# Kernel tuning notes

Measured on AMD Instinct MI355X. Metric: run time of the kernel, lower is better.

Reference implementation:

```python
import jax, jax.numpy as jnp
import numpy as np

N = 50000   # num nodes
E = 800000  # num edges
D = 128     # embedding dim
EPS = 1e-5


def setup_inputs() -> dict:
    key = jax.random.key(0)
    ks = jax.random.split(key, 16)
    x = jnp.arange(N, dtype=jnp.int32)
    edge_index = jax.random.randint(ks[0], (2, E), 0, N, dtype=jnp.int32)
    weight = jax.random.uniform(ks[1], (E,), dtype=jnp.float32)
    emb = jax.random.normal(ks[2], (N, D), dtype=jnp.float32)
    # layer dims: 128->128, 128->64, 64->32
    dims = [(128, 128), (128, 64), (64, 32)]
    inp = {"x": x, "edge_index": edge_index, "weight": weight, "emb": emb}
    for i, (fi, fo) in enumerate(dims, start=1):
        s = 1.0 / np.sqrt(fi)
        inp[f"W{i}"] = jax.random.uniform(ks[3 * i], (fi, fo), dtype=jnp.float32, minval=-s, maxval=s)
        inp[f"b{i}"] = jnp.zeros((fo,), dtype=jnp.float32)
        inp[f"g{i}"] = jnp.ones((fo,), dtype=jnp.float32)
        inp[f"be{i}"] = jnp.zeros((fo,), dtype=jnp.float32)
    return inp


def _gcn_conv(h, src, dst, w, W, b):
    # PyG GCNConv: linear, add self-loops (weight 1), symmetric normalization, scatter-add
    h = h @ W  # [N, Fout]
    loop = jnp.arange(N, dtype=src.dtype)
    src_l = jnp.concatenate([src, loop])
    dst_l = jnp.concatenate([dst, loop])
    w_l = jnp.concatenate([w, jnp.ones((N,), w.dtype)])
    deg = jax.ops.segment_sum(w_l, dst_l, num_segments=N)
    dinv = jnp.where(deg > 0, jax.lax.rsqrt(jnp.maximum(deg, 1e-30)), 0.0)
    norm = dinv[src_l] * w_l * dinv[dst_l]  # [E+N]
    msg = h[src_l] * norm[:, None]          # gather + scale, [E+N, Fout]
    out = jax.ops.segment_sum(msg, dst_l, num_segments=N)
    return out + b


def _batch_norm(h, g, be):
    mu = h.mean(axis=0)
    var = h.var(axis=0)  # biased, as torch BN uses for normalization
    return (h - mu) * jax.lax.rsqrt(var + EPS) * g + be


def reference(x, edge_index, weight, emb,
              W1, b1, g1, be1,
              W2, b2, g2, be2,
              W3, b3, g3, be3):
    src, dst = edge_index[0], edge_index[1]
    h = emb[x]  # embedding lookup
    h = _batch_norm(_gcn_conv(h, src, dst, weight, W1, b1), g1, be1)
    h = jax.nn.relu(h)
    h = _batch_norm(_gcn_conv(h, src, dst, weight, W2, b2), g2, be2)
    h = jax.nn.relu(h)
    h = _batch_norm(_gcn_conv(h, src, dst, weight, W3, b3), g3, be3)
    return h
```

## Files before the change

kernel.cpp:

```cpp
#include <hip/hip_runtime.h>
#include <hip/hip_bf16.h>

#define BN_EPS 1e-5f
#define FIXSCALE 16777216.0f
#define FIXINV   5.9604644775390625e-08
#define LOWMASK  0xFFFFFFFFFFULL

typedef __attribute__((ext_vector_type(8))) short bf16x8;
typedef __attribute__((ext_vector_type(4))) float f32x4;

__device__ __forceinline__ unsigned short bfu(float v) {
  return __bfloat16_as_ushort(__float2bfloat16(v));
}
__device__ __forceinline__ unsigned int pk_bf2(float a, float b) {
  return (unsigned int)bfu(a) | ((unsigned int)bfu(b) << 16);
}
__device__ __forceinline__ float bf_lo(unsigned int u) { return __uint_as_float(u << 16); }
__device__ __forceinline__ float bf_hi(unsigned int u) { return __uint_as_float(u & 0xFFFF0000u); }

__device__ __forceinline__ void fma8(float* a, uint4 u, float c) {
  a[0] += bf_lo(u.x) * c; a[1] += bf_hi(u.x) * c;
  a[2] += bf_lo(u.y) * c; a[3] += bf_hi(u.y) * c;
  a[4] += bf_lo(u.z) * c; a[5] += bf_hi(u.z) * c;
  a[6] += bf_lo(u.w) * c; a[7] += bf_hi(u.w) * c;
}

__device__ __forceinline__ float4 load4(const float* p) { return *(const float4*)p; }
__device__ __forceinline__ float4 load4(const unsigned short* p) {
  uint2 u = *(const uint2*)p;
  return make_float4(bf_lo(u.x), bf_hi(u.x), bf_lo(u.y), bf_hi(u.y));
}


__global__ void prep_k(const float* __restrict__ W1, const float* __restrict__ W2,
                       const float* __restrict__ W3, unsigned short* __restrict__ wt1,
                       unsigned short* __restrict__ wt2, unsigned short* __restrict__ wt3,
                       unsigned long long* __restrict__ packed, int n) {
  int idx = blockIdx.x * 256 + threadIdx.x;
  if (idx < n) packed[idx] = 0ULL;
  if (idx < 128 * 128) {
    int c = idx >> 7, k = idx & 127;
    wt1[idx] = bfu(W1[k * 128 + c]);
  } else if (idx < 128 * 128 + 128 * 64) {
    int i2 = idx - 128 * 128;
    int c = i2 >> 7, k = i2 & 127;
    wt2[i2] = bfu(W2[k * 64 + c]);
  } else if (idx < 128 * 128 + 128 * 64 + 64 * 32) {
    int i2 = idx - 128 * 128 - 128 * 64;
    int c = i2 >> 6, k = i2 & 63;
    wt3[i2] = bfu(W3[k * 32 + c]);
  }
}


__global__ void hist64_k(const int* __restrict__ dst, const float* __restrict__ w,
                         unsigned long long* __restrict__ packed, int* __restrict__ rank, int e) {
  int i = blockIdx.x * blockDim.x + threadIdx.x;
  if (i < e) {
    unsigned long long fw = (unsigned long long)__float2uint_rn(w[i] * FIXSCALE);
    unsigned long long old = atomicAdd(&packed[dst[i]], (1ULL << 40) | fw);
    rank[i] = (int)(old >> 40);
  }
}

__global__ void scan_partial_k(const unsigned long long* __restrict__ packed,
                               int* __restrict__ bsum, float* __restrict__ dinv, int n) {
  __shared__ int s[256];
  int idx = blockIdx.x * 256 + threadIdx.x;
  unsigned long long p = (idx < n) ? packed[idx] : 0ULL;
  if (idx < n)
    dinv[idx] = rsqrtf(1.0f + (float)((double)(p & LOWMASK) * FIXINV));
  s[threadIdx.x] = (int)(p >> 40);
  __syncthreads();
  for (int off = 128; off > 0; off >>= 1) {
    if (threadIdx.x < off) s[threadIdx.x] += s[threadIdx.x + off];
    __syncthreads();
  }
  if (threadIdx.x == 0) bsum[blockIdx.x] = s[0];
}

__global__ void scan_tops_k(int* __restrict__ bsum, int* __restrict__ total_out, int nb) {
  __shared__ int s[256];
  int t = threadIdx.x;
  int v = (t < nb) ? bsum[t] : 0;
  s[t] = v;
  __syncthreads();
  for (int off = 1; off < 256; off <<= 1) {
    int u = (t >= off) ? s[t - off] : 0;
    __syncthreads();
    s[t] += u;
    __syncthreads();
  }
  if (t < nb) bsum[t] = s[t] - v;
  if (t == 255) *total_out = s[255];
}

__global__ void scan_final_k(const unsigned long long* __restrict__ packed,
                             const int* __restrict__ bsum, int* __restrict__ rowptr, int n) {
  __shared__ int s[256];
  int b = blockIdx.x, t = threadIdx.x;
  int idx = b * 256 + t;
  int v = (idx < n) ? (int)(packed[idx] >> 40) : 0;
  s[t] = v;
  __syncthreads();
  for (int off = 1; off < 256; off <<= 1) {
    int u = (t >= off) ? s[t - off] : 0;
    __syncthreads();
    s[t] += u;
    __syncthreads();
  }
  if (idx < n) rowptr[idx] = bsum[b] + s[t] - v;
}

__global__ void scatter_nb_k(const int* __restrict__ src, const int* __restrict__ dst,
                             const float* __restrict__ w, const int* __restrict__ rank,
                             const float* __restrict__ dinv, const int* __restrict__ rowptr,
                             int2* __restrict__ csr, int e) {
  int i = blockIdx.x * blockDim.x + threadIdx.x;
  if (i < e) {
    int d = dst[i], s = src[i];
    int pos = rowptr[d] + rank[i];
    float c = dinv[s] * w[i] * dinv[d];
    csr[pos] = make_int2(s, __float_as_int(c));
  }
}


template <typename TIN, int FIN, int FOUT, bool BNIN, bool GATHER, bool TILEOUT>
__global__ __launch_bounds__(256) void gemm_mfma_k(
    const TIN* __restrict__ H, const int* __restrict__ xidx,
    const float* __restrict__ scale, const float* __restrict__ shift,
    const unsigned short* __restrict__ WtG, unsigned short* __restrict__ out, int n) {
  constexpr int C4 = FIN / 4;
  constexpr int ldH = FIN + 8;
  constexpr int ldW = FIN + 8;
  constexpr int ldC = FOUT + 4;
  constexpr int NCT = FOUT / 16;
  constexpr int NK = FIN / 32;
  constexpr int HT_SH = 64 * ldH;
  constexpr int WT_SH = FOUT * ldW;
  constexpr int STAGE_B = (HT_SH + WT_SH) * 2;
  constexpr int C_B = 64 * ldC * 4;
  constexpr int BYTES = STAGE_B > C_B ? STAGE_B : C_B;

  __shared__ __align__(16) char smem[BYTES];
  unsigned short* Ht = (unsigned short*)smem;
  unsigned short* Wt = (unsigned short*)smem + HT_SH;
  float* Cs = (float*)smem;

  const int t = threadIdx.x;
  const int r0 = blockIdx.x * 64;

  constexpr int NH = 64 * C4 / 256;
#pragma unroll
  for (int i = 0; i < NH; ++i) {
    int idx = t + 256 * i;
    int r = idx / C4, c4 = idx % C4;
    int gr = r0 + r;
    if (gr < n) {
      int srow = GATHER ? xidx[gr] : gr;
      float4 v = load4(H + (size_t)srow * FIN + c4 * 4);
      if (BNIN) {
        float4 sc = *(const float4*)(scale + c4 * 4);
        float4 sh = *(const float4*)(shift + c4 * 4);
        v.x = fmaxf(v.x * sc.x + sh.x, 0.f);
        v.y = fmaxf(v.y * sc.y + sh.y, 0.f);
        v.z = fmaxf(v.z * sc.z + sh.z, 0.f);
        v.w = fmaxf(v.w * sc.w + sh.w, 0.f);
      }
      ushort4 p;
      p.x = bfu(v.x); p.y = bfu(v.y); p.z = bfu(v.z); p.w = bfu(v.w);
      *(ushort4*)&Ht[r * ldH + c4 * 4] = p;
    }
  }
  constexpr int NWU = FOUT * FIN / 8 / 256;
#pragma unroll
  for (int i = 0; i < NWU; ++i) {
    int idx = t + 256 * i;
    int wr = idx / (FIN / 8), w8 = idx % (FIN / 8);
    *(uint4*)&Wt[wr * ldW + w8 * 8] = *(const uint4*)&WtG[wr * FIN + w8 * 8];
  }
  __syncthreads();

  const int w = t >> 6;
  const int l = t & 63;
  const int l15 = l & 15;
  const int kg = l >> 4;
  const int arow = w * 16 + l15;

  f32x4 acc[NCT];
#pragma unroll
  for (int c = 0; c < NCT; ++c) acc[c] = (f32x4){0.f, 0.f, 0.f, 0.f};

#pragma unroll
  for (int kk = 0; kk < NK; ++kk) {
    bf16x8 a = *(const bf16x8*)&Ht[arow * ldH + kk * 32 + kg * 8];
#pragma unroll
    for (int c = 0; c < NCT; ++c) {
      bf16x8 b = *(const bf16x8*)&Wt[(c * 16 + l15) * ldW + kk * 32 + kg * 8];
      acc[c] = __builtin_amdgcn_mfma_f32_16x16x32_bf16(a, b, acc[c], 0, 0, 0);
    }
  }
  __syncthreads();

#pragma unroll
  for (int c = 0; c < NCT; ++c)
#pragma unroll
    for (int m = 0; m < 4; ++m)
      Cs[(w * 16 + kg * 4 + m) * ldC + c * 16 + l15] = acc[c][m];
  __syncthreads();

  constexpr int NU = 64 * FOUT / 8 / 256;
#pragma unroll
  for (int i = 0; i < NU; ++i) {
    int u = t + 256 * i;
    int r = u / (FOUT / 8), c8 = u % (FOUT / 8);
    int gr = r0 + r;
    if (gr < n) {
      const float* p = &Cs[r * ldC + c8 * 8];
      float4 v0 = *(const float4*)p;
      float4 v1 = *(const float4*)(p + 4);
      uint4 o;
      o.x = pk_bf2(v0.x, v0.y); o.y = pk_bf2(v0.z, v0.w);
      o.z = pk_bf2(v1.x, v1.y); o.w = pk_bf2(v1.z, v1.w);
      if (TILEOUT) {
        *(uint4*)&out[((size_t)(c8 >> 2) * n + gr) * 32 + (c8 & 3) * 8] = o;
      } else {
        *(uint4*)&out[(size_t)gr * FOUT + c8 * 8] = o;
      }
    }
  }
}


__global__ __launch_bounds__(256) void agg_csr_t_k(
    const unsigned short* __restrict__ hWt, const int* __restrict__ rowptr,
    const int2* __restrict__ csr, const float* __restrict__ dinv,
    const float* __restrict__ b, unsigned short* __restrict__ out, int n) {
  const int bid = blockIdx.x;
  const int xcd = bid & 7;
  const int tile = xcd >> 1;
  const int row0 = (bid >> 3) * 128 + (xcd & 1) * 64;
  const int t = threadIdx.x;
  const int j = t & 3;
  const int row = row0 + (t >> 2);
  if (row >= n) return;

  const unsigned short* base = hWt + (size_t)tile * n * 32;
  const float di = dinv[row];
  const float c0 = di * di;
  float a[8];
  {
    uint4 hu = *(const uint4*)(base + (size_t)row * 32 + j * 8);
    const float4 bb0 = *(const float4*)(b + tile * 32 + j * 8);
    const float4 bb1 = *(const float4*)(b + tile * 32 + j * 8 + 4);
    a[0] = bb0.x; a[1] = bb0.y; a[2] = bb0.z; a[3] = bb0.w;
    a[4] = bb1.x; a[5] = bb1.y; a[6] = bb1.z; a[7] = bb1.w;
    fma8(a, hu, c0);
  }

  const int e0 = rowptr[row], e1 = rowptr[row + 1];
  int ee = e0;
  for (; ee + 1 < e1; ee += 2) {
    const int2 d0 = csr[ee];
    const int2 d1 = csr[ee + 1];
    const uint4 u0 = *(const uint4*)(base + (size_t)d0.x * 32 + j * 8);
    const uint4 u1 = *(const uint4*)(base + (size_t)d1.x * 32 + j * 8);
    fma8(a, u0, __int_as_float(d0.y));
    fma8(a, u1, __int_as_float(d1.y));
  }
  if (ee < e1) {
    const int2 d0 = csr[ee];
    const uint4 u0 = *(const uint4*)(base + (size_t)d0.x * 32 + j * 8);
    fma8(a, u0, __int_as_float(d0.y));
  }

  uint4 o;
  o.x = pk_bf2(a[0], a[1]); o.y = pk_bf2(a[2], a[3]);
  o.z = pk_bf2(a[4], a[5]); o.w = pk_bf2(a[6], a[7]);
  *(uint4*)&out[(size_t)row * 128 + tile * 32 + j * 8] = o;
}


template <int FOUT>
__global__ void agg_csr_k(const unsigned short* __restrict__ hW, const int* __restrict__ rowptr,
                          const int2* __restrict__ csr, const float* __restrict__ dinv,
                          const float* __restrict__ b, unsigned short* __restrict__ out, int n) {
  constexpr int TPR = FOUT / 8;
  int gid = blockIdx.x * blockDim.x + threadIdx.x;
  int row = gid / TPR, j = gid % TPR;
  if (row >= n) return;

  const float di = dinv[row];
  const float c0 = di * di;
  float a[8];
  {
    uint4 hu = *(const uint4*)(hW + (size_t)row * FOUT + j * 8);
    const float4 bb0 = *(const float4*)(b + j * 8);
    const float4 bb1 = *(const float4*)(b + j * 8 + 4);
    a[0] = bb0.x; a[1] = bb0.y; a[2] = bb0.z; a[3] = bb0.w;
    a[4] = bb1.x; a[5] = bb1.y; a[6] = bb1.z; a[7] = bb1.w;
    fma8(a, hu, c0);
  }

  const int e0 = rowptr[row], e1 = rowptr[row + 1];
  int ee = e0;
  for (; ee + 1 < e1; ee += 2) {
    const int2 d0 = csr[ee];
    const int2 d1 = csr[ee + 1];
    const uint4 u0 = *(const uint4*)(hW + (size_t)d0.x * FOUT + j * 8);
    const uint4 u1 = *(const uint4*)(hW + (size_t)d1.x * FOUT + j * 8);
    fma8(a, u0, __int_as_float(d0.y));
    fma8(a, u1, __int_as_float(d1.y));
  }
  if (ee < e1) {
    const int2 d0 = csr[ee];
    const uint4 u0 = *(const uint4*)(hW + (size_t)d0.x * FOUT + j * 8);
    fma8(a, u0, __int_as_float(d0.y));
  }

  uint4 o;
  o.x = pk_bf2(a[0], a[1]); o.y = pk_bf2(a[2], a[3]);
  o.z = pk_bf2(a[4], a[5]); o.w = pk_bf2(a[6], a[7]);
  *(uint4*)&out[(size_t)row * FOUT + j * 8] = o;
}


template <int FOUT>
__global__ __launch_bounds__(256) void bn_stats_part_k(
    const unsigned short* __restrict__ h, float* __restrict__ psum,
    float* __restrict__ psq, int n) {
  constexpr int TPR = FOUT / 8;
  constexpr int RPB = 256 / TPR;
  const int t = threadIdx.x;
  const int j = t % TPR;
  const int rp = t / TPR;

  float s[8] = {0.f, 0.f, 0.f, 0.f, 0.f, 0.f, 0.f, 0.f};
  float q[8] = {0.f, 0.f, 0.f, 0.f, 0.f, 0.f, 0.f, 0.f};
  for (int r = blockIdx.x * RPB + rp; r < n; r += gridDim.x * RPB) {
    uint4 u = *(const uint4*)(h + (size_t)r * FOUT + j * 8);
    float v[8] = {bf_lo(u.x), bf_hi(u.x), bf_lo(u.y), bf_hi(u.y),
                  bf_lo(u.z), bf_hi(u.z), bf_lo(u.w), bf_hi(u.w)};
#pragma unroll
    for (int k = 0; k < 8; ++k) { s[k] += v[k]; q[k] += v[k] * v[k]; }
  }

  __shared__ float4 ls0[256], ls1[256], lq0[256], lq1[256];
  ls0[t] = make_float4(s[0], s[1], s[2], s[3]);
  ls1[t] = make_float4(s[4], s[5], s[6], s[7]);
  lq0[t] = make_float4(q[0], q[1], q[2], q[3]);
  lq1[t] = make_float4(q[4], q[5], q[6], q[7]);
  __syncthreads();
#pragma unroll
  for (int off = RPB / 2; off > 0; off >>= 1) {
    if (rp < off) {
      int o = off * TPR;
      float4 a, b2;
      a = ls0[t]; b2 = ls0[t + o]; ls0[t] = make_float4(a.x + b2.x, a.y + b2.y, a.z + b2.z, a.w + b2.w);
      a = ls1[t]; b2 = ls1[t + o]; ls1[t] = make_float4(a.x + b2.x, a.y + b2.y, a.z + b2.z, a.w + b2.w);
      a = lq0[t]; b2 = lq0[t + o]; lq0[t] = make_float4(a.x + b2.x, a.y + b2.y, a.z + b2.z, a.w + b2.w);
      a = lq1[t]; b2 = lq1[t + o]; lq1[t] = make_float4(a.x + b2.x, a.y + b2.y, a.z + b2.z, a.w + b2.w);
    }
    __syncthreads();
  }
  if (rp == 0) {
    *(float4*)&psum[(size_t)blockIdx.x * FOUT + j * 8] = ls0[j];
    *(float4*)&psum[(size_t)blockIdx.x * FOUT + j * 8 + 4] = ls1[j];
    *(float4*)&psq[(size_t)blockIdx.x * FOUT + j * 8] = lq0[j];
    *(float4*)&psq[(size_t)blockIdx.x * FOUT + j * 8 + 4] = lq1[j];
  }
}

template <int FOUT>
__global__ __launch_bounds__(256) void bn_finalize2_k(
    const float* __restrict__ psum, const float* __restrict__ psq,
    const float* __restrict__ g, const float* __restrict__ be,
    float* __restrict__ scale, float* __restrict__ shift, int nb, int n) {
  constexpr int TPR = FOUT / 4;
  constexpr int GR = 256 / TPR;
  const int t = threadIdx.x;
  const int j = t % TPR;
  const int gr = t / TPR;

  float4 s = make_float4(0.f, 0.f, 0.f, 0.f);
  float4 q = make_float4(0.f, 0.f, 0.f, 0.f);
  for (int b = gr; b < nb; b += GR) {
    float4 v = *(const float4*)&psum[(size_t)b * FOUT + j * 4];
    float4 u = *(const float4*)&psq[(size_t)b * FOUT + j * 4];
    s.x += v.x; s.y += v.y; s.z += v.z; s.w += v.w;
    q.x += u.x; q.y += u.y; q.z += u.z; q.w += u.w;
  }
  __shared__ float4 ls[256];
  __shared__ float4 lq[256];
  ls[t] = s;
  lq[t] = q;
  __syncthreads();
#pragma unroll
  for (int off = GR / 2; off > 0; off >>= 1) {
    if (gr < off) {
      float4 a = ls[t], b2 = ls[t + off * TPR];
      ls[t] = make_float4(a.x + b2.x, a.y + b2.y, a.z + b2.z, a.w + b2.w);
      float4 c = lq[t], d = lq[t + off * TPR];
      lq[t] = make_float4(c.x + d.x, c.y + d.y, c.z + d.z, c.w + d.w);
    }
    __syncthreads();
  }
  if (gr == 0) {
    float4 s4 = ls[j], q4 = lq[j];
    float inv_n = 1.0f / (float)n;
    float mu[4] = {s4.x * inv_n, s4.y * inv_n, s4.z * inv_n, s4.w * inv_n};
    float qq[4] = {q4.x, q4.y, q4.z, q4.w};
#pragma unroll
    for (int k = 0; k < 4; ++k) {
      int c = j * 4 + k;
      float var = qq[k] * inv_n - mu[k] * mu[k];
      float sc = g[c] * rsqrtf(var + BN_EPS);
      scale[c] = sc;
      shift[c] = be[c] - mu[k] * sc;
    }
  }
}

__global__ void bn_apply32_k(const unsigned short* __restrict__ in,
                             const float* __restrict__ scale, const float* __restrict__ shift,
                             float* __restrict__ out, int n) {
  int gid = blockIdx.x * blockDim.x + threadIdx.x;
  int row = gid >> 2, j = gid & 3;
  if (row >= n) return;
  uint4 u = *(const uint4*)(in + (size_t)row * 32 + j * 8);
  float v[8] = {bf_lo(u.x), bf_hi(u.x), bf_lo(u.y), bf_hi(u.y),
                bf_lo(u.z), bf_hi(u.z), bf_lo(u.w), bf_hi(u.w)};
  const float4 sc0 = *(const float4*)(scale + j * 8);
  const float4 sc1 = *(const float4*)(scale + j * 8 + 4);
  const float4 sh0 = *(const float4*)(shift + j * 8);
  const float4 sh1 = *(const float4*)(shift + j * 8 + 4);
  float4 o0 = make_float4(v[0] * sc0.x + sh0.x, v[1] * sc0.y + sh0.y,
                          v[2] * sc0.z + sh0.z, v[3] * sc0.w + sh0.w);
  float4 o1 = make_float4(v[4] * sc1.x + sh1.x, v[5] * sc1.y + sh1.y,
                          v[6] * sc1.z + sh1.z, v[7] * sc1.w + sh1.w);
  float* p = out + (size_t)row * 32 + j * 8;
  *(float4*)p = o0;
  *(float4*)(p + 4) = o1;
}


static inline size_t pad4(size_t v) { return (v + 3) & ~(size_t)3; }

extern "C" void kernel_launch(void* const* d_in, const int* in_sizes, int n_in,
                              void* d_out, int out_size, void* d_ws, size_t ws_size,
                              hipStream_t stream) {
  const int* x = (const int*)d_in[0];
  const int* ei = (const int*)d_in[1];
  const float* w = (const float*)d_in[2];
  const float* emb = (const float*)d_in[3];
  const float* W1 = (const float*)d_in[4];
  const float* b1 = (const float*)d_in[5];
  const float* g1 = (const float*)d_in[6];
  const float* be1 = (const float*)d_in[7];
  const float* W2 = (const float*)d_in[8];
  const float* b2 = (const float*)d_in[9];
  const float* g2 = (const float*)d_in[10];
  const float* be2 = (const float*)d_in[11];
  const float* W3 = (const float*)d_in[12];
  const float* b3 = (const float*)d_in[13];
  const float* g3 = (const float*)d_in[14];
  const float* be3 = (const float*)d_in[15];

  const int n = in_sizes[0];
  const int e = in_sizes[2];
  const int* src = ei;
  const int* dst = ei + e;

  float* ws = (float*)d_ws;
  size_t off = 0;
  unsigned short* bufA16 = (unsigned short*)(ws + off); off += pad4((size_t)n * 64);
  unsigned short* bufB16 = (unsigned short*)(ws + off); off += pad4((size_t)n * 64);
  unsigned long long* packed = (unsigned long long*)(ws + off); off += pad4((size_t)n * 2);
  float* dinv = ws + off; off += pad4(n);
  int* rowptr = (int*)(ws + off); off += pad4(n + 1);
  int* rank = (int*)(ws + off); off += pad4(e);
  int2* csr = (int2*)(ws + off); off += pad4((size_t)e * 2);
  unsigned short* wt1 = (unsigned short*)(ws + off); off += 128 * 128 / 2;
  unsigned short* wt2 = (unsigned short*)(ws + off); off += 128 * 64 / 2;
  unsigned short* wt3 = (unsigned short*)(ws + off); off += 64 * 32 / 2;
  float* psum = ws + off; off += 256 * 128;
  float* psq = ws + off; off += 256 * 128;
  float* scale = ws + off; off += 128;
  float* shift = ws + off; off += 128;
  int* bsum = (int*)(ws + off); off += 256;

  const int B = 256;
  dim3 blk(B);
  const int nb = (n + 255) / 256;
  const int SB = 256;

  prep_k<<<(n + B - 1) / B, blk, 0, stream>>>(W1, W2, W3, wt1, wt2, wt3, packed, n);
  hist64_k<<<(e + B - 1) / B, blk, 0, stream>>>(dst, w, packed, rank, e);
  scan_partial_k<<<nb, blk, 0, stream>>>(packed, bsum, dinv, n);
  scan_tops_k<<<1, blk, 0, stream>>>(bsum, rowptr + n, nb);
  scan_final_k<<<nb, blk, 0, stream>>>(packed, bsum, rowptr, n);
  scatter_nb_k<<<(e + B - 1) / B, blk, 0, stream>>>(src, dst, w, rank, dinv, rowptr, csr, e);

  const int gx = (n + 63) / 64;

  gemm_mfma_k<float, 128, 128, false, true, true><<<gx, blk, 0, stream>>>(emb, x, nullptr, nullptr, wt1, bufA16, n);
  agg_csr_t_k<<<((n + 127) / 128) * 8, blk, 0, stream>>>(bufA16, rowptr, csr, dinv, b1, bufB16, n);
  bn_stats_part_k<128><<<SB, blk, 0, stream>>>(bufB16, psum, psq, n);
  bn_finalize2_k<128><<<1, blk, 0, stream>>>(psum, psq, g1, be1, scale, shift, SB, n);

  gemm_mfma_k<unsigned short, 128, 64, true, false, false><<<gx, blk, 0, stream>>>(bufB16, nullptr, scale, shift, wt2, bufA16, n);
  agg_csr_k<64><<<((size_t)n * 8 + B - 1) / B, blk, 0, stream>>>(bufA16, rowptr, csr, dinv, b2, bufB16, n);
  bn_stats_part_k<64><<<SB, blk, 0, stream>>>(bufB16, psum, psq, n);
  bn_finalize2_k<64><<<1, blk, 0, stream>>>(psum, psq, g2, be2, scale, shift, SB, n);

  gemm_mfma_k<unsigned short, 64, 32, true, false, false><<<gx, blk, 0, stream>>>(bufB16, nullptr, scale, shift, wt3, bufA16, n);
  agg_csr_k<32><<<((size_t)n * 4 + B - 1) / B, blk, 0, stream>>>(bufA16, rowptr, csr, dinv, b3, bufB16, n);
  bn_stats_part_k<32><<<SB, blk, 0, stream>>>(bufB16, psum, psq, n);
  bn_finalize2_k<32><<<1, blk, 0, stream>>>(psum, psq, g3, be3, scale, shift, SB, n);
  bn_apply32_k<<<((size_t)n * 4 + B - 1) / B, blk, 0, stream>>>(bufB16, scale, shift, (float*)d_out, n);
}
```

Before: 213.9 us.

## Fuse scan and BN finalize kernels, vectorize edge kernels, drop tiled layer-1 aggregation

Merges the top-level block-sum scan into scan_final_k and folds the BN finalize step into the stats kernel through a last-block atomic counter, removing four kernel launches. The histogram and scatter kernels now handle two edges per thread with vector loads. Layer 1 drops the XCD-tiled 32-column aggregation layout and uses the generic row-major agg_csr_k<128>. Together these aim to cut launch overhead and per-edge load count, at the risk of losing the L2 locality that the tiled layout was built for.

```diff
diff --git a/kernel.cpp b/kernel.cpp
--- a/kernel.cpp
+++ b/kernel.cpp
@@ -35,9 +35,10 @@
 __global__ void prep_k(const float* __restrict__ W1, const float* __restrict__ W2,
                        const float* __restrict__ W3, unsigned short* __restrict__ wt1,
                        unsigned short* __restrict__ wt2, unsigned short* __restrict__ wt3,
-                       unsigned long long* __restrict__ packed, int n) {
+                       unsigned long long* __restrict__ packed, int* __restrict__ ctr, int n) {
   int idx = blockIdx.x * 256 + threadIdx.x;
   if (idx < n) packed[idx] = 0ULL;
+  if (idx == 0) *ctr = 0;
   if (idx < 128 * 128) {
     int c = idx >> 7, k = idx & 127;
     wt1[idx] = bfu(W1[k * 128 + c]);
@@ -55,8 +56,16 @@
 
 __global__ void hist64_k(const int* __restrict__ dst, const float* __restrict__ w,
                          unsigned long long* __restrict__ packed, int* __restrict__ rank, int e) {
-  int i = blockIdx.x * blockDim.x + threadIdx.x;
-  if (i < e) {
+  int i = (blockIdx.x * blockDim.x + threadIdx.x) * 2;
+  if (i + 1 < e) {
+    int2 d2 = *(const int2*)(dst + i);
+    float2 w2 = *(const float2*)(w + i);
+    unsigned long long a0 = (1ULL << 40) | (unsigned long long)__float2uint_rn(w2.x * FIXSCALE);
+    unsigned long long a1 = (1ULL << 40) | (unsigned long long)__float2uint_rn(w2.y * FIXSCALE);
+    unsigned long long o0 = atomicAdd(&packed[d2.x], a0);
+    unsigned long long o1 = atomicAdd(&packed[d2.y], a1);
+    *(int2*)(rank + i) = make_int2((int)(o0 >> 40), (int)(o1 >> 40));
+  } else if (i < e) {
     unsigned long long fw = (unsigned long long)__float2uint_rn(w[i] * FIXSCALE);
     unsigned long long old = atomicAdd(&packed[dst[i]], (1ULL << 40) | fw);
     rank[i] = (int)(old >> 40);
@@ -79,26 +88,25 @@
   if (threadIdx.x == 0) bsum[blockIdx.x] = s[0];
 }
 
-__global__ void scan_tops_k(int* __restrict__ bsum, int* __restrict__ total_out, int nb) {
+__global__ void scan_final_k(const unsigned long long* __restrict__ packed,
+                             const int* __restrict__ bsum, int* __restrict__ rowptr,
+                             int n, int nb) {
+  __shared__ int sb[256];
   __shared__ int s[256];
-  int t = threadIdx.x;
-  int v = (t < nb) ? bsum[t] : 0;
-  s[t] = v;
+  const int b = blockIdx.x, t = threadIdx.x;
+
+  int bv = (t < nb) ? bsum[t] : 0;
+  sb[t] = bv;
   __syncthreads();
   for (int off = 1; off < 256; off <<= 1) {
-    int u = (t >= off) ? s[t - off] : 0;
-    __syncthreads();
-    s[t] += u;
-    __syncthreads();
-  }
-  if (t < nb) bsum[t] = s[t] - v;
-  if (t == 255) *total_out = s[255];
-}
-
-__global__ void scan_final_k(const unsigned long long* __restrict__ packed,
-                             const int* __restrict__ bsum, int* __restrict__ rowptr, int n) {
-  __shared__ int s[256];
-  int b = blockIdx.x, t = threadIdx.x;
+    int u = (t >= off) ? sb[t - off] : 0;
+    __syncthreads();
+    sb[t] += u;
+    __syncthreads();
+  }
+  const int blockbase = (b == 0) ? 0 : sb[b - 1];
+  if (b == 0 && t == 0) rowptr[n] = sb[nb - 1];
+
   int idx = b * 256 + t;
   int v = (idx < n) ? (int)(packed[idx] >> 40) : 0;
   s[t] = v;
@@ -109,24 +117,32 @@
     s[t] += u;
     __syncthreads();
   }
-  if (idx < n) rowptr[idx] = bsum[b] + s[t] - v;
+  if (idx < n) rowptr[idx] = blockbase + s[t] - v;
 }
 
 __global__ void scatter_nb_k(const int* __restrict__ src, const int* __restrict__ dst,
                              const float* __restrict__ w, const int* __restrict__ rank,
                              const float* __restrict__ dinv, const int* __restrict__ rowptr,
                              int2* __restrict__ csr, int e) {
-  int i = blockIdx.x * blockDim.x + threadIdx.x;
-  if (i < e) {
+  int i = (blockIdx.x * blockDim.x + threadIdx.x) * 2;
+  if (i + 1 < e) {
+    int2 s2 = *(const int2*)(src + i);
+    int2 d2 = *(const int2*)(dst + i);
+    float2 w2 = *(const float2*)(w + i);
+    int2 r2 = *(const int2*)(rank + i);
+    int p0 = rowptr[d2.x] + r2.x;
+    int p1 = rowptr[d2.y] + r2.y;
+    csr[p0] = make_int2(s2.x, __float_as_int(dinv[s2.x] * w2.x * dinv[d2.x]));
+    csr[p1] = make_int2(s2.y, __float_as_int(dinv[s2.y] * w2.y * dinv[d2.y]));
+  } else if (i < e) {
     int d = dst[i], s = src[i];
     int pos = rowptr[d] + rank[i];
-    float c = dinv[s] * w[i] * dinv[d];
-    csr[pos] = make_int2(s, __float_as_int(c));
-  }
-}
-
-
-template <typename TIN, int FIN, int FOUT, bool BNIN, bool GATHER, bool TILEOUT>
+    csr[pos] = make_int2(s, __float_as_int(dinv[s] * w[i] * dinv[d]));
+  }
+}
+
+
+template <typename TIN, int FIN, int FOUT, bool BNIN, bool GATHER>
 __global__ __launch_bounds__(256) void gemm_mfma_k(
     const TIN* __restrict__ H, const int* __restrict__ xidx,
     const float* __restrict__ scale, const float* __restrict__ shift,
@@ -223,62 +239,9 @@
       uint4 o;
       o.x = pk_bf2(v0.x, v0.y); o.y = pk_bf2(v0.z, v0.w);
       o.z = pk_bf2(v1.x, v1.y); o.w = pk_bf2(v1.z, v1.w);
-      if (TILEOUT) {
-        *(uint4*)&out[((size_t)(c8 >> 2) * n + gr) * 32 + (c8 & 3) * 8] = o;
-      } else {
-        *(uint4*)&out[(size_t)gr * FOUT + c8 * 8] = o;
-      }
-    }
-  }
-}
-
-
-__global__ __launch_bounds__(256) void agg_csr_t_k(
-    const unsigned short* __restrict__ hWt, const int* __restrict__ rowptr,
-    const int2* __restrict__ csr, const float* __restrict__ dinv,
-    const float* __restrict__ b, unsigned short* __restrict__ out, int n) {
-  const int bid = blockIdx.x;
-  const int xcd = bid & 7;
-  const int tile = xcd >> 1;
-  const int row0 = (bid >> 3) * 128 + (xcd & 1) * 64;
-  const int t = threadIdx.x;
-  const int j = t & 3;
-  const int row = row0 + (t >> 2);
-  if (row >= n) return;
-
-  const unsigned short* base = hWt + (size_t)tile * n * 32;
-  const float di = dinv[row];
-  const float c0 = di * di;
-  float a[8];
-  {
-    uint4 hu = *(const uint4*)(base + (size_t)row * 32 + j * 8);
-    const float4 bb0 = *(const float4*)(b + tile * 32 + j * 8);
-    const float4 bb1 = *(const float4*)(b + tile * 32 + j * 8 + 4);
-    a[0] = bb0.x; a[1] = bb0.y; a[2] = bb0.z; a[3] = bb0.w;
-    a[4] = bb1.x; a[5] = bb1.y; a[6] = bb1.z; a[7] = bb1.w;
-    fma8(a, hu, c0);
-  }
-
-  const int e0 = rowptr[row], e1 = rowptr[row + 1];
-  int ee = e0;
-  for (; ee + 1 < e1; ee += 2) {
-    const int2 d0 = csr[ee];
-    const int2 d1 = csr[ee + 1];
-    const uint4 u0 = *(const uint4*)(base + (size_t)d0.x * 32 + j * 8);
-    const uint4 u1 = *(const uint4*)(base + (size_t)d1.x * 32 + j * 8);
-    fma8(a, u0, __int_as_float(d0.y));
-    fma8(a, u1, __int_as_float(d1.y));
-  }
-  if (ee < e1) {
-    const int2 d0 = csr[ee];
-    const uint4 u0 = *(const uint4*)(base + (size_t)d0.x * 32 + j * 8);
-    fma8(a, u0, __int_as_float(d0.y));
-  }
-
-  uint4 o;
-  o.x = pk_bf2(a[0], a[1]); o.y = pk_bf2(a[2], a[3]);
-  o.z = pk_bf2(a[4], a[5]); o.w = pk_bf2(a[6], a[7]);
-  *(uint4*)&out[(size_t)row * 128 + tile * 32 + j * 8] = o;
+      *(uint4*)&out[(size_t)gr * FOUT + c8 * 8] = o;
+    }
+  }
 }
 
 
@@ -327,9 +290,10 @@
 
 
 template <int FOUT>
-__global__ __launch_bounds__(256) void bn_stats_part_k(
-    const unsigned short* __restrict__ h, float* __restrict__ psum,
-    float* __restrict__ psq, int n) {
+__global__ __launch_bounds__(256) void bn_stats_fin_k(
+    const unsigned short* __restrict__ h, float* __restrict__ psum, float* __restrict__ psq,
+    const float* __restrict__ g, const float* __restrict__ be,
+    float* __restrict__ scale, float* __restrict__ shift, int* __restrict__ ctr, int n) {
   constexpr int TPR = FOUT / 8;
   constexpr int RPB = 256 / TPR;
   const int t = threadIdx.x;
@@ -347,6 +311,7 @@
   }
 
   __shared__ float4 ls0[256], ls1[256], lq0[256], lq1[256];
+  __shared__ int lastflag;
   ls0[t] = make_float4(s[0], s[1], s[2], s[3]);
   ls1[t] = make_float4(s[4], s[5], s[6], s[7]);
   lq0[t] = make_float4(q[0], q[1], q[2], q[3]);
@@ -370,56 +335,53 @@
     *(float4*)&psq[(size_t)blockIdx.x * FOUT + j * 8] = lq0[j];
     *(float4*)&psq[(size_t)blockIdx.x * FOUT + j * 8 + 4] = lq1[j];
   }
-}
-
-template <int FOUT>
-__global__ __launch_bounds__(256) void bn_finalize2_k(
-    const float* __restrict__ psum, const float* __restrict__ psq,
-    const float* __restrict__ g, const float* __restrict__ be,
-    float* __restrict__ scale, float* __restrict__ shift, int nb, int n) {
-  constexpr int TPR = FOUT / 4;
-  constexpr int GR = 256 / TPR;
-  const int t = threadIdx.x;
-  const int j = t % TPR;
-  const int gr = t / TPR;
-
-  float4 s = make_float4(0.f, 0.f, 0.f, 0.f);
-  float4 q = make_float4(0.f, 0.f, 0.f, 0.f);
-  for (int b = gr; b < nb; b += GR) {
-    float4 v = *(const float4*)&psum[(size_t)b * FOUT + j * 4];
-    float4 u = *(const float4*)&psq[(size_t)b * FOUT + j * 4];
-    s.x += v.x; s.y += v.y; s.z += v.z; s.w += v.w;
-    q.x += u.x; q.y += u.y; q.z += u.z; q.w += u.w;
-  }
-  __shared__ float4 ls[256];
-  __shared__ float4 lq[256];
-  ls[t] = s;
-  lq[t] = q;
+  __threadfence();
+  if (t == 0) lastflag = (atomicAdd(ctr, 1) == (int)gridDim.x - 1);
+  __syncthreads();
+  if (!lastflag) return;
+
+  constexpr int TPR4 = FOUT / 4;
+  constexpr int GR = 256 / TPR4;
+  const int j4 = t % TPR4;
+  const int gr = t / TPR4;
+  float4 ss = make_float4(0.f, 0.f, 0.f, 0.f);
+  float4 qq = make_float4(0.f, 0.f, 0.f, 0.f);
+  for (int b = gr; b < (int)gridDim.x; b += GR) {
+    float4 v = *(const float4*)&psum[(size_t)b * FOUT + j4 * 4];
+    float4 u = *(const float4*)&psq[(size_t)b * FOUT + j4 * 4];
+    ss.x += v.x; ss.y += v.y; ss.z += v.z; ss.w += v.w;
+    qq.x += u.x; qq.y += u.y; qq.z += u.z; qq.w += u.w;
+  }
+  __syncthreads();
+  ls0[t] = ss;
+  lq0[t] = qq;
   __syncthreads();
 #pragma unroll
   for (int off = GR / 2; off > 0; off >>= 1) {
     if (gr < off) {
-      float4 a = ls[t], b2 = ls[t + off * TPR];
-      ls[t] = make_float4(a.x + b2.x, a.y + b2.y, a.z + b2.z, a.w + b2.w);
-      float4 c = lq[t], d = lq[t + off * TPR];
-      lq[t] = make_float4(c.x + d.x, c.y + d.y, c.z + d.z, c.w + d.w);
+      int o = off * TPR4;
+      float4 a = ls0[t], b2 = ls0[t + o];
+      ls0[t] = make_float4(a.x + b2.x, a.y + b2.y, a.z + b2.z, a.w + b2.w);
+      float4 c = lq0[t], d = lq0[t + o];
+      lq0[t] = make_float4(c.x + d.x, c.y + d.y, c.z + d.z, c.w + d.w);
     }
     __syncthreads();
   }
   if (gr == 0) {
-    float4 s4 = ls[j], q4 = lq[j];
+    float4 s4 = ls0[j4], q4 = lq0[j4];
     float inv_n = 1.0f / (float)n;
     float mu[4] = {s4.x * inv_n, s4.y * inv_n, s4.z * inv_n, s4.w * inv_n};
-    float qq[4] = {q4.x, q4.y, q4.z, q4.w};
+    float qv[4] = {q4.x, q4.y, q4.z, q4.w};
 #pragma unroll
     for (int k = 0; k < 4; ++k) {
-      int c = j * 4 + k;
-      float var = qq[k] * inv_n - mu[k] * mu[k];
+      int c = j4 * 4 + k;
+      float var = qv[k] * inv_n - mu[k] * mu[k];
       float sc = g[c] * rsqrtf(var + BN_EPS);
       scale[c] = sc;
       shift[c] = be[c] - mu[k] * sc;
     }
   }
+  if (t == 0) atomicExch(ctr, 0);
 }
 
 __global__ void bn_apply32_k(const unsigned short* __restrict__ in,
@@ -489,34 +451,32 @@
   float* scale = ws + off; off += 128;
   float* shift = ws + off; off += 128;
   int* bsum = (int*)(ws + off); off += 256;
+  int* ctr = (int*)(ws + off); off += 4;
 
   const int B = 256;
   dim3 blk(B);
   const int nb = (n + 255) / 256;
+  const int e2 = (e + 1) / 2;
   const int SB = 256;
 
-  prep_k<<<(n + B - 1) / B, blk, 0, stream>>>(W1, W2, W3, wt1, wt2, wt3, packed, n);
-  hist64_k<<<(e + B - 1) / B, blk, 0, stream>>>(dst, w, packed, rank, e);
+  prep_k<<<(n + B - 1) / B, blk, 0, stream>>>(W1, W2, W3, wt1, wt2, wt3, packed, ctr, n);
+  hist64_k<<<(e2 + B - 1) / B, blk, 0, stream>>>(dst, w, packed, rank, e);
   scan_partial_k<<<nb, blk, 0, stream>>>(packed, bsum, dinv, n);
-  scan_tops_k<<<1, blk, 0, stream>>>(bsum, rowptr + n, nb);
-  scan_final_k<<<nb, blk, 0, stream>>>(packed, bsum, rowptr, n);
-  scatter_nb_k<<<(e + B - 1) / B, blk, 0, stream>>>(src, dst, w, rank, dinv, rowptr, csr, e);
+  scan_final_k<<<nb, blk, 0, stream>>>(packed, bsum, rowptr, n, nb);
+  scatter_nb_k<<<(e2 + B - 1) / B, blk, 0, stream>>>(src, dst, w, rank, dinv, rowptr, csr, e);
 
   const int gx = (n + 63) / 64;
 
-  gemm_mfma_k<float, 128, 128, false, true, true><<<gx, blk, 0, stream>>>(emb, x, nullptr, nullptr, wt1, bufA16, n);
-  agg_csr_t_k<<<((n + 127) / 128) * 8, blk, 0, stream>>>(bufA16, rowptr, csr, dinv, b1, bufB16, n);
-  bn_stats_part_k<128><<<SB, blk, 0, stream>>>(bufB16, psum, psq, n);
-  bn_finalize2_k<128><<<1, blk, 0, stream>>>(psum, psq, g1, be1, scale, shift, SB, n);
-
-  gemm_mfma_k<unsigned short, 128, 64, true, false, false><<<gx, blk, 0, stream>>>(bufB16, nullptr, scale, shift, wt2, bufA16, n);
+  gemm_mfma_k<float, 128, 128, false, true><<<gx, blk, 0, stream>>>(emb, x, nullptr, nullptr, wt1, bufA16, n);
+  agg_csr_k<128><<<((size_t)n * 16 + B - 1) / B, blk, 0, stream>>>(bufA16, rowptr, csr, dinv, b1, bufB16, n);
+  bn_stats_fin_k<128><<<SB, blk, 0, stream>>>(bufB16, psum, psq, g1, be1, scale, shift, ctr, n);
+
+  gemm_mfma_k<unsigned short, 128, 64, true, false><<<gx, blk, 0, stream>>>(bufB16, nullptr, scale, shift, wt2, bufA16, n);
   agg_csr_k<64><<<((size_t)n * 8 + B - 1) / B, blk, 0, stream>>>(bufA16, rowptr, csr, dinv, b2, bufB16, n);
-  bn_stats_part_k<64><<<SB, blk, 0, stream>>>(bufB16, psum, psq, n);
-  bn_finalize2_k<64><<<1, blk, 0, stream>>>(psum, psq, g2, be2, scale, shift, SB, n);
-
-  gemm_mfma_k<unsigned short, 64, 32, true, false, false><<<gx, blk, 0, stream>>>(bufB16, nullptr, scale, shift, wt3, bufA16, n);
+  bn_stats_fin_k<64><<<SB, blk, 0, stream>>>(bufB16, psum, psq, g2, be2, scale, shift, ctr, n);
+
+  gemm_mfma_k<unsigned short, 64, 32, true, false><<<gx, blk, 0, stream>>>(bufB16, nullptr, scale, shift, wt3, bufA16, n);
   agg_csr_k<32><<<((size_t)n * 4 + B - 1) / B, blk, 0, stream>>>(bufA16, rowptr, csr, dinv, b3, bufB16, n);
-  bn_stats_part_k<32><<<SB, blk, 0, stream>>>(bufB16, psum, psq, n);
-  bn_finalize2_k<32><<<1, blk, 0, stream>>>(psum, psq, g3, be3, scale, shift, SB, n);
+  bn_stats_fin_k<32><<<SB, blk, 0, stream>>>(bufB16, psum, psq, g3, be3, scale, shift, ctr, n);
   bn_apply32_k<<<((size_t)n * 4 + B - 1) / B, blk, 0, stream>>>(bufB16, scale, shift, (float*)d_out, n);
 }
```

New measurement: 254.4 us. +19.0%, slower.
